# Kernel tuning notes

Measured on AMD Instinct MI355X. Metric: run time of the kernel, lower is better.

Reference implementation:

```python
import jax, jax.numpy as jnp
import numpy as np

B, N, D = 8, 8192, 64          # batch, input points, point feature dim
NPOINT, NSAMPLE = 1024, 16     # FPS samples S, KNN neighbors K
WN, OUT = 16, 128              # weightnet out channels, output channels
CIN = 3 + D                    # concat(xyz_norm, point feats) = linear in_channel
NEG_SLOPE = 0.1


def setup_inputs() -> dict:
    key = jax.random.key(0)
    ks = jax.random.split(key, 8)
    rn = lambda k, shp, s: jax.random.normal(k, shp, jnp.float32) * s
    return {
        "xyz": rn(ks[0], (B, 3, N), 1.0),
        "points": rn(ks[1], (B, D, N), 1.0),
        "w1": rn(ks[2], (3, 8), 0.5), "b1": jnp.zeros((8,), jnp.float32),
        "w2": rn(ks[3], (8, 8), 0.35), "b2": jnp.zeros((8,), jnp.float32),
        "w3": rn(ks[4], (8, WN), 0.35), "b3": jnp.zeros((WN,), jnp.float32),
        "lin_w": rn(ks[5], (WN * CIN, OUT), 0.03),
        "lin_b": jnp.zeros((OUT,), jnp.float32),
    }


def _fps(xyz):
    """Furthest point sampling. xyz: [B,N,3] -> idx [B,NPOINT] int32."""
    def step(carry, _):
        dist, farthest = carry  # [B,N], [B]
        centroid = jnp.take_along_axis(xyz, farthest[:, None, None], axis=1)  # [B,1,3]
        d = jnp.sum((xyz - centroid) ** 2, axis=-1)  # [B,N]
        dist = jnp.minimum(dist, d)
        return (dist, jnp.argmax(dist, axis=-1).astype(jnp.int32)), farthest
    init = (jnp.full((xyz.shape[0], xyz.shape[1]), 1e10, xyz.dtype),
            jnp.zeros((xyz.shape[0],), jnp.int32))
    _, idxs = jax.lax.scan(step, init, None, length=NPOINT)
    return idxs.T  # [B, NPOINT]


def reference(xyz, points, w1, b1, w2, b2, w3, b3, lin_w, lin_b):
    xyz_t = xyz.transpose(0, 2, 1)       # [B,N,3]
    pts_t = points.transpose(0, 2, 1)    # [B,N,D]

    fps_idx = _fps(xyz_t)                                   # [B,S]
    bidx = jnp.arange(B)[:, None]
    new_xyz = xyz_t[bidx, fps_idx]                          # [B,S,3]

    # KNN: squared distances (same ordering as euclidean cdist)
    sqr = jnp.sum((new_xyz[:, :, None, :] - xyz_t[:, None, :, :]) ** 2, axis=-1)  # [B,S,N]
    _, knn = jax.lax.top_k(-sqr, NSAMPLE)                   # [B,S,K]

    b3i = jnp.arange(B)[:, None, None]
    g_xyz = xyz_t[b3i, knn]                                 # [B,S,K,3]
    g_xyz_norm = g_xyz - new_xyz[:, :, None, :]             # [B,S,K,3]
    g_pts = pts_t[b3i, knn]                                 # [B,S,K,D]
    feat = jnp.concatenate([g_xyz_norm, g_pts], axis=-1)    # [B,S,K,3+D]

    # WeightNet: 1x1 convs == per-neighbor MLP on xyz offsets
    h = jax.nn.relu(g_xyz_norm @ w1 + b1)
    h = jax.nn.relu(h @ w2 + b2)
    wts = jax.nn.relu(h @ w3 + b3)                          # [B,S,K,WN]

    # weighted aggregation over K, then flatten [C, WN]
    agg = jnp.einsum('bskc,bskw->bscw', feat, wts).reshape(B, NPOINT, CIN * WN)
    out = agg @ lin_w + lin_b                               # [B,S,OUT]
    out = jnp.where(out > 0, out, NEG_SLOPE * out)          # LeakyReLU(0.1)

    return new_xyz.transpose(0, 2, 1), out.transpose(0, 2, 1), fps_idx
```

## Files before the change

kernel.cpp:

```cpp
#include <hip/hip_runtime.h>
#include <hip/hip_bf16.h>

#define NPTS   8192
#define NBATCH 8
#define S      1024
#define K      16
#define D      64
#define CIN    67
#define WN     16
#define OUTC   128

#define OUT_MAIN 24576
#define OUT_FPS  1073152

template <int CTRL, int RM>
__device__ __forceinline__ unsigned long long dpp_max_step(unsigned long long key) {
  int lo = __builtin_amdgcn_update_dpp(0, (int)(unsigned)(key & 0xFFFFFFFFull), CTRL, RM, 0xF, true);
  int hi = __builtin_amdgcn_update_dpp(0, (int)(unsigned)(key >> 32),           CTRL, RM, 0xF, true);
  unsigned long long o = ((unsigned long long)(unsigned)hi << 32) | (unsigned)lo;
  return o > key ? o : key;
}

__global__ __launch_bounds__(256)
void stage0_kernel(const float* __restrict__ xyz, const float* __restrict__ pts,
                   float* __restrict__ newxyz, float* __restrict__ ptt,
                   float* __restrict__ out)
{
#pragma clang fp contract(off)
  __shared__ float s_x[NPTS], s_y[NPTS], s_z[NPTS];
  __shared__ float4 hist[1024];
  __shared__ unsigned long long slots[2][4];

  if (blockIdx.x >= 8) {
    const int bid = blockIdx.x - 8;
    const int b   = bid >> 7;
    const int n0  = (bid & 127) * 64;
    const float* pb = pts + (size_t)b * D * NPTS;
#pragma unroll
    for (int i = 0; i < 16; i++) {
      int s = threadIdx.x + i * 256;
      int nl = s & 63, d = s >> 6;
      s_x[d * 65 + nl] = pb[(size_t)d * NPTS + n0 + nl];
    }
    __syncthreads();
    float* ob = ptt + ((size_t)b * NPTS + n0) * D;
#pragma unroll
    for (int i = 0; i < 16; i++) {
      int s = threadIdx.x + i * 256;
      int dl = s & 63, nl = s >> 6;
      ob[(size_t)nl * D + dl] = s_x[dl * 65 + nl];
    }
    return;
  }

  const int b    = blockIdx.x;
  const int tid  = threadIdx.x;
  const int wave = tid >> 6;
  const int lane = tid & 63;
  const float* xb = xyz + (size_t)b * 3 * NPTS;

  float px[32], py[32], pz[32], dist[32];
#pragma unroll
  for (int i = 0; i < 32; i++) {
    int n = i * 256 + tid;
    px[i] = xb[n];
    py[i] = xb[NPTS + n];
    pz[i] = xb[2 * NPTS + n];
    dist[i] = 1e10f;
    s_x[n] = px[i]; s_y[n] = py[i]; s_z[n] = pz[i];
  }

  int far = 0;
  float cx = xb[0], cy = xb[NPTS], cz = xb[2 * NPTS];

  for (int t = 0; t < 1024; t++) {
    if (tid == (t & 255))
      hist[t] = make_float4(cx, cy, cz, (float)far);

    float bd = -1.0f; int bi = 0;
#pragma unroll
    for (int i = 0; i < 32; i++) {
      float dx = px[i] - cx, dy = py[i] - cy, dz = pz[i] - cz;
      float d  = (dx * dx + dy * dy) + dz * dz;
      float nd = fminf(dist[i], d);
      dist[i] = nd;
      if (nd > bd) { bd = nd; bi = i * 256 + tid; }
    }

    unsigned long long key =
        ((unsigned long long)__float_as_uint(bd) << 32) | (unsigned)(~(unsigned)bi);
    key = dpp_max_step<0x111, 0xF>(key);
    key = dpp_max_step<0x112, 0xF>(key);
    key = dpp_max_step<0x114, 0xF>(key);
    key = dpp_max_step<0x118, 0xF>(key);
    key = dpp_max_step<0x142, 0xA>(key);
    key = dpp_max_step<0x143, 0xC>(key);
    if (lane == 63) slots[t & 1][wave] = key;
    __syncthreads();

    unsigned long long k0 = slots[t & 1][0], k1 = slots[t & 1][1];
    unsigned long long k2 = slots[t & 1][2], k3 = slots[t & 1][3];
    k0 = k1 > k0 ? k1 : k0;
    k2 = k3 > k2 ? k3 : k2;
    k0 = k2 > k0 ? k2 : k0;
    int gi = (int)(~(unsigned)(k0 & 0xFFFFFFFFull));
    far = gi;
    cx = s_x[gi]; cy = s_y[gi]; cz = s_z[gi];
  }
  __syncthreads();

#pragma unroll
  for (int j = 0; j < 4; j++) {
    int t = j * 256 + tid;
    float4 h = hist[t];
    out[OUT_FPS + b * 1024 + t] = h.w;
    out[b * 3072 + t]           = h.x;
    out[b * 3072 + 1024 + t]    = h.y;
    out[b * 3072 + 2048 + t]    = h.z;
    newxyz[(b * 1024 + t) * 3 + 0] = h.x;
    newxyz[(b * 1024 + t) * 3 + 1] = h.y;
    newxyz[(b * 1024 + t) * 3 + 2] = h.z;
  }
}

__global__ __launch_bounds__(256)
void knn_kernel(const float* __restrict__ xyz, const float* __restrict__ newxyz,
                int* __restrict__ knn)
{
#pragma clang fp contract(off)
  __shared__ unsigned long long s_k[16][16 * 17];
  const int tid   = threadIdx.x;
  const int cl    = tid >> 4;
  const int chunk = tid & 15;
  const int csel  = blockIdx.x * 16 + cl;
  const int b     = csel >> 10;
  const float* xb = xyz + (size_t)b * 3 * NPTS;
  const float cx = newxyz[csel * 3 + 0];
  const float cy = newxyz[csel * 3 + 1];
  const float cz = newxyz[csel * 3 + 2];

  float nd[16]; int ni[16];
#pragma unroll
  for (int k = 0; k < 16; k++) { nd[k] = 3.4e38f; ni[k] = 0x7FFFFFFF; }

  for (int jj = 0; jj < 512; jj++) {
    int j = jj * 16 + chunk;
    float dx = xb[j] - cx, dy = xb[NPTS + j] - cy, dz = xb[2 * NPTS + j] - cz;
    float d  = (dx * dx + dy * dy) + dz * dz;
    float cv = d; int iv = j;
#pragma unroll
    for (int k = 0; k < 16; k++) {
      bool sw = cv < nd[k];
      float tv = nd[k]; int ti = ni[k];
      nd[k] = sw ? cv : tv;  ni[k] = sw ? iv : ti;
      cv    = sw ? tv : cv;  iv    = sw ? ti : iv;
    }
  }
#pragma unroll
  for (int k = 0; k < 16; k++)
    s_k[cl][chunk * 17 + k] =
        ((unsigned long long)__float_as_uint(nd[k]) << 32) | (unsigned)ni[k];
  s_k[cl][chunk * 17 + 16] = ~0ull;
  __syncthreads();

  if (tid < 16) {
    int pos[16];
#pragma unroll
    for (int c = 0; c < 16; c++) pos[c] = 0;
    for (int r = 0; r < 16; r++) {
      unsigned long long bk = ~0ull; int bc = 0;
#pragma unroll
      for (int c = 0; c < 16; c++) {
        unsigned long long kv = s_k[tid][c * 17 + pos[c]];
        if (kv < bk) { bk = kv; bc = c; }
      }
#pragma unroll
      for (int c = 0; c < 16; c++) pos[c] += (c == bc);
      knn[(size_t)(blockIdx.x * 16 + tid) * 16 + r] = (int)(bk & 0xFFFFFFFFull);
    }
  }
}

__global__ __launch_bounds__(256)
void feat_agg_kernel(const float* __restrict__ xyz, const float* __restrict__ newxyz,
                     const float* __restrict__ ptt, const int* __restrict__ knn,
                     const float* __restrict__ w1, const float* __restrict__ b1,
                     const float* __restrict__ w2, const float* __restrict__ b2,
                     const float* __restrict__ w3, const float* __restrict__ b3,
                     float* __restrict__ agg)
{
  const int wv   = threadIdx.x >> 6;
  const int lane = threadIdx.x & 63;
  const int csel = blockIdx.x * 4 + wv;
  const int b    = csel >> 10;

  __shared__ float s_wts[4][16 * 17];
  __shared__ float s_off[4][16 * 3];
  __shared__ int   s_nk[4][16];

  if (lane < 16) {
    int nk = knn[(size_t)csel * 16 + lane];
    s_nk[wv][lane] = nk;
    const float* xb = xyz + (size_t)b * 3 * NPTS;
    float ox = xb[nk]            - newxyz[csel * 3 + 0];
    float oy = xb[NPTS + nk]     - newxyz[csel * 3 + 1];
    float oz = xb[2 * NPTS + nk] - newxyz[csel * 3 + 2];
    s_off[wv][lane * 3 + 0] = ox;
    s_off[wv][lane * 3 + 1] = oy;
    s_off[wv][lane * 3 + 2] = oz;
    float h1[8], h2[8];
#pragma unroll
    for (int j = 0; j < 8; j++)
      h1[j] = fmaxf(0.f, ox * w1[j] + oy * w1[8 + j] + oz * w1[16 + j] + b1[j]);
#pragma unroll
    for (int j = 0; j < 8; j++) {
      float a = b2[j];
#pragma unroll
      for (int i = 0; i < 8; i++) a = fmaf(h1[i], w2[i * 8 + j], a);
      h2[j] = fmaxf(0.f, a);
    }
#pragma unroll
    for (int w = 0; w < 16; w++) {
      float a = b3[w];
#pragma unroll
      for (int i = 0; i < 8; i++) a = fmaf(h2[i], w3[i * 16 + w], a);
      s_wts[wv][lane * 17 + w] = fmaxf(0.f, a);
    }
  }
  __syncthreads();

  float f[16];
#pragma unroll
  for (int k = 0; k < 16; k++) {
    int nk = s_nk[wv][k];
    f[k] = ptt[((size_t)b * NPTS + nk) * D + lane];
  }

  float acc[16];
#pragma unroll
  for (int w = 0; w < 16; w++) acc[w] = 0.f;
#pragma unroll
  for (int k = 0; k < 16; k++) {
#pragma unroll
    for (int w = 0; w < 16; w++)
      acc[w] = fmaf(f[k], s_wts[wv][k * 17 + w], acc[w]);
  }
  float* arow = agg + (size_t)csel * (CIN * WN) + (3 + lane) * 16;
#pragma unroll
  for (int q = 0; q < 4; q++) {
    float4 v = make_float4(acc[4 * q], acc[4 * q + 1], acc[4 * q + 2], acc[4 * q + 3]);
    *(float4*)(arow + 4 * q) = v;
  }

  if (lane < 48) {
    int c = lane >> 4, w = lane & 15;
    float a = 0.f;
#pragma unroll
    for (int k = 0; k < 16; k++)
      a = fmaf(s_off[wv][k * 3 + c], s_wts[wv][k * 17 + w], a);
    agg[(size_t)csel * (CIN * WN) + c * 16 + w] = a;
  }
}

__global__ __launch_bounds__(256)
void gemm_out_kernel(const float* __restrict__ agg, const float* __restrict__ lin_w,
                     const float* __restrict__ lin_b, float* __restrict__ out)
{
  __shared__ float a_t[16 * 68];
  __shared__ float b_t[16 * 64];
  const int tid  = threadIdx.x;
  const int rt   = blockIdx.x >> 1;
  const int ct   = blockIdx.x & 1;
  const int row0 = rt * 64;
  const int c0   = ct * 64;
  const int cg   = tid & 31;
  const int rg   = tid >> 5;

  float acc[8][2] = {};
  for (int kt = 0; kt < 67; kt++) {
    const int k0 = kt * 16;
#pragma unroll
    for (int i = 0; i < 4; i++) {
      int s = tid + i * 256;
      int kk = s & 15, r = s >> 4;
      a_t[kk * 68 + r] = agg[(size_t)(row0 + r) * (CIN * WN) + k0 + kk];
    }
#pragma unroll
    for (int i = 0; i < 4; i++) {
      int s = tid + i * 256;
      int c = s & 63, kk = s >> 6;
      b_t[kk * 64 + c] = lin_w[(size_t)(k0 + kk) * OUTC + c0 + c];
    }
    __syncthreads();
#pragma unroll
    for (int kk = 0; kk < 16; kk++) {
      const float4 a0 = *(const float4*)&a_t[kk * 68 + rg * 8];
      const float4 a1 = *(const float4*)&a_t[kk * 68 + rg * 8 + 4];
      float bv0 = b_t[kk * 64 + cg * 2];
      float bv1 = b_t[kk * 64 + cg * 2 + 1];
      float av[8] = {a0.x, a0.y, a0.z, a0.w, a1.x, a1.y, a1.z, a1.w};
#pragma unroll
      for (int rr = 0; rr < 8; rr++) {
        acc[rr][0] = fmaf(av[rr], bv0, acc[rr][0]);
        acc[rr][1] = fmaf(av[rr], bv1, acc[rr][1]);
      }
    }
    __syncthreads();
  }
#pragma unroll
  for (int rr = 0; rr < 8; rr++) {
#pragma unroll
    for (int cc = 0; cc < 2; cc++) {
      int R = row0 + rg * 8 + rr;
      int C = c0 + cg * 2 + cc;
      float v = acc[rr][cc] + lin_b[C];
      v = v > 0.f ? v : 0.1f * v;
      int bb = R >> 10, ss = R & 1023;
      out[OUT_MAIN + ((size_t)(bb * OUTC + C)) * 1024 + ss] = v;
    }
  }
}

extern "C" void kernel_launch(void* const* d_in, const int* in_sizes, int n_in,
                              void* d_out, int out_size, void* d_ws, size_t ws_size,
                              hipStream_t stream) {
  const float* xyz    = (const float*)d_in[0];
  const float* points = (const float*)d_in[1];
  const float* w1     = (const float*)d_in[2];
  const float* b1     = (const float*)d_in[3];
  const float* w2     = (const float*)d_in[4];
  const float* b2     = (const float*)d_in[5];
  const float* w3     = (const float*)d_in[6];
  const float* b3     = (const float*)d_in[7];
  const float* lin_w  = (const float*)d_in[8];
  const float* lin_b  = (const float*)d_in[9];
  float* out = (float*)d_out;
  char*  ws  = (char*)d_ws;

  float* newxyz = (float*)(ws);
  int*   knn    = (int*)  (ws + 98304);
  float* ptt    = (float*)(ws + 1048576);
  float* agg    = (float*)(ws + 17825792);

  stage0_kernel<<<8 + NBATCH * 128, 256, 0, stream>>>(xyz, points, newxyz, ptt, out);
  knn_kernel<<<512, 256, 0, stream>>>(xyz, newxyz, knn);
  feat_agg_kernel<<<2048, 256, 0, stream>>>(xyz, newxyz, ptt, knn,
                                            w1, b1, w2, b2, w3, b3, agg);
  gemm_out_kernel<<<256, 256, 0, stream>>>(agg, lin_w, lin_b, out);
}
```

Measured before the change: 1.393 ms.

## Widen FPS block to 512 threads and use packed float2 distance math

The FPS block grows from 256 to 512 threads (8 waves), so each thread owns 16 points instead of 32. The distance update is written with 2-wide float vectors so the compiler can emit packed FP32 instructions. Each thread keeps separate even and odd argmax trackers and merges them before the DPP wave reduction, and the cross-wave merge now covers 8 slots. This shortens the serial per-iteration critical path of the 1024-step FPS loop, at the cost of a wider barrier and a longer slot reduction each iteration.

Measured after the change: 1.365 ms. 1.02x faster.

```diff
diff --git a/kernel.cpp b/kernel.cpp
--- a/kernel.cpp
+++ b/kernel.cpp
@@ -13,6 +13,8 @@
 #define OUT_MAIN 24576
 #define OUT_FPS  1073152
 
+typedef float v2f __attribute__((ext_vector_type(2)));
+
 template <int CTRL, int RM>
 __device__ __forceinline__ unsigned long long dpp_max_step(unsigned long long key) {
   int lo = __builtin_amdgcn_update_dpp(0, (int)(unsigned)(key & 0xFFFFFFFFull), CTRL, RM, 0xF, true);
@@ -21,7 +23,7 @@
   return o > key ? o : key;
 }
 
-__global__ __launch_bounds__(256)
+__global__ __launch_bounds__(512)
 void stage0_kernel(const float* __restrict__ xyz, const float* __restrict__ pts,
                    float* __restrict__ newxyz, float* __restrict__ ptt,
                    float* __restrict__ out)
@@ -29,7 +31,7 @@
 #pragma clang fp contract(off)
   __shared__ float s_x[NPTS], s_y[NPTS], s_z[NPTS];
   __shared__ float4 hist[1024];
-  __shared__ unsigned long long slots[2][4];
+  __shared__ unsigned long long slots[2][8];
 
   if (blockIdx.x >= 8) {
     const int bid = blockIdx.x - 8;
@@ -37,16 +39,16 @@
     const int n0  = (bid & 127) * 64;
     const float* pb = pts + (size_t)b * D * NPTS;
 #pragma unroll
-    for (int i = 0; i < 16; i++) {
-      int s = threadIdx.x + i * 256;
+    for (int i = 0; i < 8; i++) {
+      int s = threadIdx.x + i * 512;
       int nl = s & 63, d = s >> 6;
       s_x[d * 65 + nl] = pb[(size_t)d * NPTS + n0 + nl];
     }
     __syncthreads();
     float* ob = ptt + ((size_t)b * NPTS + n0) * D;
 #pragma unroll
-    for (int i = 0; i < 16; i++) {
-      int s = threadIdx.x + i * 256;
+    for (int i = 0; i < 8; i++) {
+      int s = threadIdx.x + i * 512;
       int dl = s & 63, nl = s >> 6;
       ob[(size_t)nl * D + dl] = s_x[dl * 65 + nl];
     }
@@ -59,36 +61,49 @@
   const int lane = tid & 63;
   const float* xb = xyz + (size_t)b * 3 * NPTS;
 
-  float px[32], py[32], pz[32], dist[32];
-#pragma unroll
-  for (int i = 0; i < 32; i++) {
-    int n = i * 256 + tid;
-    px[i] = xb[n];
-    py[i] = xb[NPTS + n];
-    pz[i] = xb[2 * NPTS + n];
-    dist[i] = 1e10f;
-    s_x[n] = px[i]; s_y[n] = py[i]; s_z[n] = pz[i];
+  v2f px[8], py[8], pz[8], dist[8];
+#pragma unroll
+  for (int p = 0; p < 8; p++) {
+    int ne = (2 * p) * 512 + tid;
+    int no = ne + 512;
+    px[p] = (v2f){xb[ne], xb[no]};
+    py[p] = (v2f){xb[NPTS + ne], xb[NPTS + no]};
+    pz[p] = (v2f){xb[2 * NPTS + ne], xb[2 * NPTS + no]};
+    dist[p] = (v2f){1e10f, 1e10f};
+    s_x[ne] = px[p].x; s_x[no] = px[p].y;
+    s_y[ne] = py[p].x; s_y[no] = py[p].y;
+    s_z[ne] = pz[p].x; s_z[no] = pz[p].y;
   }
 
   int far = 0;
   float cx = xb[0], cy = xb[NPTS], cz = xb[2 * NPTS];
 
   for (int t = 0; t < 1024; t++) {
-    if (tid == (t & 255))
+    if (tid == (t & 511))
       hist[t] = make_float4(cx, cy, cz, (float)far);
 
-    float bd = -1.0f; int bi = 0;
-#pragma unroll
-    for (int i = 0; i < 32; i++) {
-      float dx = px[i] - cx, dy = py[i] - cy, dz = pz[i] - cz;
-      float d  = (dx * dx + dy * dy) + dz * dz;
-      float nd = fminf(dist[i], d);
-      dist[i] = nd;
-      if (nd > bd) { bd = nd; bi = i * 256 + tid; }
-    }
-
-    unsigned long long key =
-        ((unsigned long long)__float_as_uint(bd) << 32) | (unsigned)(~(unsigned)bi);
+    const v2f c2x = (v2f){cx, cx}, c2y = (v2f){cy, cy}, c2z = (v2f){cz, cz};
+
+    float bd_e = -1.0f, bd_o = -1.0f;
+    int   ce   = 0,     co   = 0;
+#pragma unroll
+    for (int p = 0; p < 8; p++) {
+      v2f dx = px[p] - c2x, dy = py[p] - c2y, dz = pz[p] - c2z;
+      v2f d  = (dx * dx + dy * dy) + dz * dz;
+      float nde = fminf(dist[p].x, d.x);
+      float ndo = fminf(dist[p].y, d.y);
+      dist[p].x = nde;
+      dist[p].y = ndo;
+      if (nde > bd_e) { bd_e = nde; ce = 2 * p; }
+      if (ndo > bd_o) { bd_o = ndo; co = 2 * p + 1; }
+    }
+
+    unsigned long long ke =
+        ((unsigned long long)__float_as_uint(bd_e) << 32) | (unsigned)(~(unsigned)(ce * 512 + tid));
+    unsigned long long ko =
+        ((unsigned long long)__float_as_uint(bd_o) << 32) | (unsigned)(~(unsigned)(co * 512 + tid));
+    unsigned long long key = ko > ke ? ko : ke;
+
     key = dpp_max_step<0x111, 0xF>(key);
     key = dpp_max_step<0x112, 0xF>(key);
     key = dpp_max_step<0x114, 0xF>(key);
@@ -100,9 +115,15 @@
 
     unsigned long long k0 = slots[t & 1][0], k1 = slots[t & 1][1];
     unsigned long long k2 = slots[t & 1][2], k3 = slots[t & 1][3];
+    unsigned long long k4 = slots[t & 1][4], k5 = slots[t & 1][5];
+    unsigned long long k6 = slots[t & 1][6], k7 = slots[t & 1][7];
     k0 = k1 > k0 ? k1 : k0;
     k2 = k3 > k2 ? k3 : k2;
+    k4 = k5 > k4 ? k5 : k4;
+    k6 = k7 > k6 ? k7 : k6;
     k0 = k2 > k0 ? k2 : k0;
+    k4 = k6 > k4 ? k6 : k4;
+    k0 = k4 > k0 ? k4 : k0;
     int gi = (int)(~(unsigned)(k0 & 0xFFFFFFFFull));
     far = gi;
     cx = s_x[gi]; cy = s_y[gi]; cz = s_z[gi];
@@ -110,8 +131,8 @@
   __syncthreads();
 
 #pragma unroll
-  for (int j = 0; j < 4; j++) {
-    int t = j * 256 + tid;
+  for (int j = 0; j < 2; j++) {
+    int t = j * 512 + tid;
     float4 h = hist[t];
     out[OUT_FPS + b * 1024 + t] = h.w;
     out[b * 3072 + t]           = h.x;
@@ -342,7 +363,7 @@
   float* ptt    = (float*)(ws + 1048576);
   float* agg    = (float*)(ws + 17825792);
 
-  stage0_kernel<<<8 + NBATCH * 128, 256, 0, stream>>>(xyz, points, newxyz, ptt, out);
+  stage0_kernel<<<8 + NBATCH * 128, 512, 0, stream>>>(xyz, points, newxyz, ptt, out);
   knn_kernel<<<512, 256, 0, stream>>>(xyz, newxyz, knn);
   feat_agg_kernel<<<2048, 256, 0, stream>>>(xyz, newxyz, ptt, knn,
                                             w1, b1, w2, b2, w3, b3, agg);
```
